# Kernel tuning notes

Hardware: AMD Instinct MI355X
Metric: run time of the kernel (lower is better)

## Reference

```python
import jax, jax.numpy as jnp
import numpy as np

N, E, IN_FT, OUT_FT = 8192, 4096, 512, 512
DENSITY = 0.02


def setup_inputs() -> dict:
    key = jax.random.key(0)
    k1, k2, k3, k4 = jax.random.split(key, 4)
    x = jax.random.normal(k1, (N, IN_FT), dtype=jnp.float32)
    hypergraph = (jax.random.uniform(k2, (N, E)) < DENSITY).astype(jnp.float32)
    # kaiming_uniform on [in, out]: fan_in = in_ft (torch fan of a Linear-style 2D param is dim 1 size? torch computes fan_in = size(1) for 2D -> out_ft here)
    bound_w = float(np.sqrt(6.0 / OUT_FT))  # kaiming_uniform a=sqrt(5)? default a=0 -> gain sqrt(2); bound = gain*sqrt(3/fan_in)
    bound_w = float(np.sqrt(2.0) * np.sqrt(3.0 / OUT_FT))
    weight = jax.random.uniform(k3, (IN_FT, OUT_FT), minval=-bound_w, maxval=bound_w, dtype=jnp.float32)
    bound_v = float(np.sqrt(2.0) * np.sqrt(3.0 / 1.0))
    V = jax.random.uniform(k4, (IN_FT, 1), minval=-bound_v, maxval=bound_v, dtype=jnp.float32)
    bias = jnp.zeros((OUT_FT,), dtype=jnp.float32)
    return {"x": x, "hypergraph": hypergraph, "weight": weight, "V": V, "bias": bias}


def reference(x, hypergraph, weight, V, bias):
    # edge embeddings: H^T @ x  -> [E, in_ft]
    edge_emb = hypergraph.T @ x
    hw = jax.nn.sigmoid(edge_emb @ V)          # [E, 1] learned hyperedge weights
    w = hw[:, 0]                                # [E]
    deg_v = (hypergraph @ hw)[:, 0]             # [N]  (sum over last dim of H @ hw)
    deg_e = jnp.sum(hypergraph, axis=0)         # [E]
    # adj = diag(deg_v) @ H @ diag(w) @ diag(deg_e) @ H^T @ diag(deg_v)
    # fused as broadcasted row/col scalings around two GEMMs (same math, no NxN)
    out = x @ weight                            # [N, out_ft]
    t = hypergraph.T @ (deg_v[:, None] * out)   # [E, out_ft]
    t = (w * deg_e)[:, None] * t                # diagonal edge scalings
    out = deg_v[:, None] * (hypergraph @ t)     # [N, out_ft]
    out = out + bias
    return (out, w)
```

## Files before the change

kernel.cpp:

```cpp
#include <hip/hip_runtime.h>


#define N_NODES 8192
#define N_EDGES 4096
#define FT 512

typedef short bf16x8 __attribute__((ext_vector_type(8)));
typedef float f32x4 __attribute__((ext_vector_type(4)));
typedef unsigned short u16;
typedef unsigned int u32;

__device__ __forceinline__ u16 f2b(float f) {
    union { float f; u32 u; } v; v.f = f;
    u32 r = v.u + 0x7FFFu + ((v.u >> 16) & 1u);
    return (u16)(r >> 16);
}
__device__ __forceinline__ float b2f(u16 h) {
    union { u32 u; float f; } v; v.u = ((u32)h) << 16; return v.f;
}


__global__ __launch_bounds__(256) void zero_kernel(float* p, int n) {
    int i = blockIdx.x * 256 + threadIdx.x;
    if (i < n) p[i] = 0.f;
}

__global__ __launch_bounds__(256) void xv_xb_kernel(const float* __restrict__ x,
                                                    const float* __restrict__ V,
                                                    float* __restrict__ xv,
                                                    u16* __restrict__ xb) {
    int row = blockIdx.x * 4 + (threadIdx.x >> 6);
    int lane = threadIdx.x & 63;
    const float* xr = x + (size_t)row * FT + lane * 8;
    const float* vr = V + lane * 8;
    float4 a0 = *(const float4*)xr, a1 = *(const float4*)(xr + 4);
    float4 b0 = *(const float4*)vr, b1 = *(const float4*)(vr + 4);
    float acc = a0.x * b0.x + a0.y * b0.y + a0.z * b0.z + a0.w * b0.w +
                a1.x * b1.x + a1.y * b1.y + a1.z * b1.z + a1.w * b1.w;
    u16 tmp[8] = {f2b(a0.x), f2b(a0.y), f2b(a0.z), f2b(a0.w),
                  f2b(a1.x), f2b(a1.y), f2b(a1.z), f2b(a1.w)};
    *(uint4*)(xb + (size_t)row * FT + lane * 8) = *(uint4*)tmp;
#pragma unroll
    for (int off = 32; off; off >>= 1) acc += __shfl_down(acc, off);
    if (lane == 0) xv[row] = acc;
}

__global__ __launch_bounds__(256) void prep_h4_kernel(const float* __restrict__ H,
                                                      const float* __restrict__ xv,
                                                      u16* __restrict__ Hbf,
                                                      u16* __restrict__ HTbf,
                                                      float* __restrict__ zsum,
                                                      float* __restrict__ desum) {
    __shared__ u32 Wt[64][33];
    __shared__ float xvs[64];
    const int t = threadIdx.x;
    const int e0 = blockIdx.x * 64, n0 = blockIdx.y * 64;
    if (t < 64) xvs[t] = xv[n0 + t];
    const int n_ld = t >> 2, seg = t & 3;
    u32 o[8];
    {
        const float* src = H + (size_t)(n0 + n_ld) * N_EDGES + e0 + seg * 16;
#pragma unroll
        for (int j = 0; j < 4; j++) {
            float4 h = *(const float4*)(src + j * 4);
            o[2 * j]     = (h.x != 0.f ? 0x3F80u : 0u) | (h.y != 0.f ? 0x3F800000u : 0u);
            o[2 * j + 1] = (h.z != 0.f ? 0x3F80u : 0u) | (h.w != 0.f ? 0x3F800000u : 0u);
        }
#pragma unroll
        for (int j = 0; j < 8; j++) Wt[n_ld][seg * 8 + j] = o[j];
    }
    __syncthreads();
    {
        u16* hdst = Hbf + (size_t)(n0 + n_ld) * N_EDGES + e0 + seg * 16;
        *(uint4*)hdst       = *(uint4*)&o[0];
        *(uint4*)(hdst + 8) = *(uint4*)&o[4];
    }
    {
        int e = t >> 2, g = t & 3;
        int ew = e >> 1;
        u32 sel = (e & 1) ? 0x07060302u : 0x05040100u;
        u32 oo[8];
        float z = 0.f, d = 0.f;
#pragma unroll
        for (int j = 0; j < 8; j++) {
            int np = g * 8 + j;
            oo[j] = __builtin_amdgcn_perm(Wt[2 * np + 1][ew], Wt[2 * np][ew], sel);
            z += (oo[j] & 0xFFFFu) ? xvs[2 * np] : 0.f;
            d += (oo[j] & 0xFFFFu) ? 1.f : 0.f;
            z += (oo[j] >> 16) ? xvs[2 * np + 1] : 0.f;
            d += (oo[j] >> 16) ? 1.f : 0.f;
        }
        u32* drow = (u32*)(HTbf + (size_t)(e0 + e) * N_NODES + n0);
        *(uint4*)(drow + g * 8)     = *(uint4*)&oo[0];
        *(uint4*)(drow + g * 8 + 4) = *(uint4*)&oo[4];
        z += __shfl_down(z, 2); z += __shfl_down(z, 1);
        d += __shfl_down(d, 2); d += __shfl_down(d, 1);
        if (g == 0) {
            atomicAdd(zsum + e0 + e, z);
            atomicAdd(desum + e0 + e, d);
        }
    }
}

__global__ __launch_bounds__(256) void sigmoid_kernel(const float* __restrict__ zsum,
                                                      const float* __restrict__ desum,
                                                      float* __restrict__ w_out,
                                                      float* __restrict__ wde) {
    int e = blockIdx.x * 256 + threadIdx.x;
    float z = zsum[e];
    float wv = 1.f / (1.f + expf(-z));
    w_out[e] = wv;
    wde[e] = wv * desum[e];
}

__global__ __launch_bounds__(256) void degv_kernel(const u16* __restrict__ Hbf,
                                                   const float* __restrict__ w,
                                                   float* __restrict__ degv) {
    int row = blockIdx.x * 4 + (threadIdx.x >> 6);
    int lane = threadIdx.x & 63;
    const uint4* hr = (const uint4*)(Hbf + (size_t)row * N_EDGES);
    float acc = 0.f;
#pragma unroll
    for (int i = 0; i < 8; i++) {
        int idx = i * 64 + lane;
        uint4 h = hr[idx];
        const float* w8 = w + idx * 8;
        float4 wa = *(const float4*)w8, wb = *(const float4*)(w8 + 4);
        acc += (h.x & 0xFFFFu) ? wa.x : 0.f;  acc += (h.x >> 16) ? wa.y : 0.f;
        acc += (h.y & 0xFFFFu) ? wa.z : 0.f;  acc += (h.y >> 16) ? wa.w : 0.f;
        acc += (h.z & 0xFFFFu) ? wb.x : 0.f;  acc += (h.z >> 16) ? wb.y : 0.f;
        acc += (h.w & 0xFFFFu) ? wb.z : 0.f;  acc += (h.w >> 16) ? wb.w : 0.f;
    }
#pragma unroll
    for (int off = 32; off; off >>= 1) acc += __shfl_down(acc, off);
    if (lane == 0) degv[row] = acc;
}

__global__ void wt_kernel(const float* __restrict__ src, u16* __restrict__ dst) {
    __shared__ float tile[32][33];
    int tx = threadIdx.x, ty = threadIdx.y;
    int c = blockIdx.x * 32 + tx;
    int r0 = blockIdx.y * 32;
#pragma unroll
    for (int i = 0; i < 4; i++)
        tile[ty + i * 8][tx] = src[(size_t)(r0 + ty + i * 8) * FT + c];
    __syncthreads();
#pragma unroll
    for (int i = 0; i < 4; i++)
        dst[(size_t)(blockIdx.x * 32 + ty + i * 8) * FT + r0 + tx] = f2b(tile[tx][ty + i * 8]);
}

__global__ void t2t_kernel(const u16* __restrict__ P, const float* __restrict__ wde,
                           u16* __restrict__ t2T) {
    __shared__ float tile[32][33];
    int tx = threadIdx.x, ty = threadIdx.y;
    int f0 = blockIdx.x * 32, e0 = blockIdx.y * 32;
#pragma unroll
    for (int i = 0; i < 4; i++) {
        int e = e0 + ty + i * 8;
        size_t idx = (size_t)e * 512 + f0 + tx;
        float s = 0.f;
#pragma unroll
        for (int sl = 0; sl < 8; sl++)
            s += b2f(P[idx + (size_t)sl * N_EDGES * 512]);
        tile[ty + i * 8][tx] = wde[e] * s;
    }
    __syncthreads();
#pragma unroll
    for (int i = 0; i < 4; i++)
        t2T[(size_t)(f0 + ty + i * 8) * N_EDGES + e0 + tx] = f2b(tile[tx][ty + i * 8]);
}

__global__ __launch_bounds__(256) void final_kernel(const u16* __restrict__ P,
                                                    const float* __restrict__ degv,
                                                    const float* __restrict__ bias,
                                                    float* __restrict__ out) {
    int i8 = blockIdx.x * 256 + threadIdx.x;
    int base = i8 * 8;
    int n = base >> 9, f = base & 511;
    float s[8] = {0.f, 0.f, 0.f, 0.f, 0.f, 0.f, 0.f, 0.f};
#pragma unroll
    for (int sl = 0; sl < 4; sl++) {
        uint4 v = *(const uint4*)(P + (size_t)sl * N_NODES * 512 + base);
        u32 ws[4] = {v.x, v.y, v.z, v.w};
#pragma unroll
        for (int j = 0; j < 4; j++) {
            s[2 * j]     += b2f((u16)(ws[j] & 0xFFFFu));
            s[2 * j + 1] += b2f((u16)(ws[j] >> 16));
        }
    }
    float dv = degv[n];
    float4 o0, o1;
    o0.x = dv * s[0] + bias[f + 0]; o0.y = dv * s[1] + bias[f + 1];
    o0.z = dv * s[2] + bias[f + 2]; o0.w = dv * s[3] + bias[f + 3];
    o1.x = dv * s[4] + bias[f + 4]; o1.y = dv * s[5] + bias[f + 5];
    o1.z = dv * s[6] + bias[f + 6]; o1.w = dv * s[7] + bias[f + 7];
    *(float4*)(out + base) = o0;
    *(float4*)(out + base + 4) = o1;
}


#define TBK 64

template <int MT, int NT, int EPI>
__global__ __launch_bounds__(256, 4)
void gemm9(const u16* __restrict__ Ap, const u16* __restrict__ Bp,
           void* __restrict__ Cp, const float* __restrict__ degv,
           int KC, int lda, int ldb, int ldc, size_t Ssz) {
    __shared__ __align__(16) u16 Alds[MT * 32 * TBK];
    __shared__ __align__(16) u16 Blds[NT * 32 * TBK];
    const int t = threadIdx.x;
    const int m0 = blockIdx.x * (MT * 32), n0 = blockIdx.y * (NT * 32);
    const int kbase = blockIdx.z * KC;
    const int wave = t >> 6, lane = t & 63, quad = lane >> 4, lo = lane & 15;
    const int wm = (wave >> 1) * (MT * 16), wn = (wave & 1) * (NT * 16);

    f32x4 acc[MT][NT];
#pragma unroll
    for (int a = 0; a < MT; a++)
#pragma unroll
        for (int b = 0; b < NT; b++) acc[a][b] = (f32x4){0.f, 0.f, 0.f, 0.f};

    for (int kk = 0; kk < KC; kk += TBK) {
        const int k0 = kbase + kk;
        __syncthreads();
#pragma unroll
        for (int i = 0; i < MT; i++) {
            int c = t + i * 256;
            int r = c >> 3;
            int j = ((c & 7) - r) & 7;
            const u16* g = Ap + (size_t)(m0 + r) * lda + k0 + j * 8;
            __builtin_amdgcn_global_load_lds((const u32*)g, (u32*)(Alds + c * 8), 16, 0, 0);
        }
#pragma unroll
        for (int i = 0; i < NT; i++) {
            int c = t + i * 256;
            int r = c >> 3;
            int j = ((c & 7) - r) & 7;
            const u16* g = Bp + (size_t)(n0 + r) * ldb + k0 + j * 8;
            __builtin_amdgcn_global_load_lds((const u32*)g, (u32*)(Blds + c * 8), 16, 0, 0);
        }
        __syncthreads();

#pragma unroll
        for (int s2 = 0; s2 < 2; s2++) {
            bf16x8 af[MT], bfr[NT];
#pragma unroll
            for (int mt = 0; mt < MT; mt++) {
                int m = wm + mt * 16 + lo;
                int s = (s2 * 4 + quad + m) & 7;
                af[mt] = *(const bf16x8*)&Alds[m * TBK + s * 8];
            }
#pragma unroll
            for (int nt = 0; nt < NT; nt++) {
                int n = wn + nt * 16 + lo;
                int s = (s2 * 4 + quad + n) & 7;
                bfr[nt] = *(const bf16x8*)&Blds[n * TBK + s * 8];
            }
#pragma unroll
            for (int mt = 0; mt < MT; mt++)
#pragma unroll
                for (int nt = 0; nt < NT; nt++)
                    acc[mt][nt] = __builtin_amdgcn_mfma_f32_16x16x32_bf16(af[mt], bfr[nt], acc[mt][nt], 0, 0, 0);
        }
    }

    if (EPI == 0) {
        u16* C = (u16*)Cp + (size_t)blockIdx.z * Ssz;
#pragma unroll
        for (int mt = 0; mt < MT; mt++) {
            int rb = m0 + wm + mt * 16 + quad * 4;
#pragma unroll
            for (int i = 0; i < 4; i++)
#pragma unroll
                for (int nt = 0; nt < NT; nt++)
                    C[(size_t)(rb + i) * ldc + n0 + wn + nt * 16 + lo] = f2b(acc[mt][nt][i]);
        }
    } else {
        u16* C = (u16*)Cp;
        float dv[NT];
#pragma unroll
        for (int nt = 0; nt < NT; nt++) dv[nt] = degv[n0 + wn + nt * 16 + lo];
#pragma unroll
        for (int mt = 0; mt < MT; mt++) {
            int rb = m0 + wm + mt * 16 + quad * 4;
#pragma unroll
            for (int i = 0; i < 4; i++)
#pragma unroll
                for (int nt = 0; nt < NT; nt++)
                    C[(size_t)(rb + i) * ldc + n0 + wn + nt * 16 + lo] =
                        f2b(acc[mt][nt][i] * dv[nt]);
        }
    }
}


extern "C" void kernel_launch(void* const* d_in, const int* in_sizes, int n_in,
                              void* d_out, int out_size, void* d_ws, size_t ws_size,
                              hipStream_t stream) {
    const float* x    = (const float*)d_in[0];
    const float* H    = (const float*)d_in[1];
    const float* W    = (const float*)d_in[2];
    const float* V    = (const float*)d_in[3];
    const float* bias = (const float*)d_in[4];
    float* out  = (float*)d_out;
    float* wout = out + (size_t)N_NODES * FT;
    (void)in_sizes; (void)n_in; (void)out_size; (void)ws_size;

    char* wsb = (char*)d_ws;
    float* wsf   = (float*)d_ws;
    float* xv    = wsf;
    float* zsum  = wsf + 8192;
    float* desum = wsf + 12288;
    float* degv  = wsf + 16384;
    float* wde   = wsf + 24576;
    u16*   Hbf   = (u16*)(wsb + 114688);
    u16*   HTbf  = (u16*)(wsb + 67223552);
    u16*   WT    = (u16*)(wsb + 134332416);
    u16*   doutT = (u16*)(wsb + 134856704);
    u16*   t2T   = (u16*)(wsb + 143245312);
    u16*   xb    = (u16*)(wsb + 147439616);
    u16*   P     = (u16*)(wsb + 155828224);

    zero_kernel<<<32, 256, 0, stream>>>(zsum, 8192);
    xv_xb_kernel<<<N_NODES / 4, 256, 0, stream>>>(x, V, xv, xb);
    prep_h4_kernel<<<dim3(N_EDGES / 64, N_NODES / 64), 256, 0, stream>>>(
        H, xv, Hbf, HTbf, zsum, desum);
    sigmoid_kernel<<<N_EDGES / 256, 256, 0, stream>>>(zsum, desum, wout, wde);
    degv_kernel<<<N_NODES / 4, 256, 0, stream>>>(Hbf, wout, degv);
    wt_kernel<<<dim3(16, 16), dim3(32, 8), 0, stream>>>(W, WT);

    gemm9<2, 4, 1><<<dim3(FT / 64, N_NODES / 128, 1), 256, 0, stream>>>(
        WT, xb, doutT, degv, FT, FT, FT, N_NODES, 0);

    gemm9<4, 4, 0><<<dim3(N_EDGES / 128, FT / 128, 8), 256, 0, stream>>>(
        HTbf, doutT, P, nullptr, N_NODES / 8, N_NODES, N_NODES, 512, (size_t)N_EDGES * 512);

    t2t_kernel<<<dim3(FT / 32, N_EDGES / 32), dim3(32, 8), 0, stream>>>(P, wde, t2T);

    gemm9<4, 4, 0><<<dim3(N_NODES / 128, FT / 128, 4), 256, 0, stream>>>(
        Hbf, t2T, P, nullptr, N_EDGES / 4, N_EDGES, N_EDGES, 512, (size_t)N_NODES * 512);

    final_kernel<<<(N_NODES * FT / 8) / 256, 256, 0, stream>>>(P, degv, bias, out);
}
```

Before: 354.3 us.

## Fuse small prep kernels and drop split-K in final GEMM with fused epilogue

Folds the zeroing into xv_xb_kernel and merges the sigmoid and weight-transpose kernels into one launch, cutting three launches. The last GEMM no longer splits K four ways into bf16 partials followed by a reduction kernel. It now runs the full K=4096 per block with a smaller 64-row tile and writes fp32 output directly with degree scaling and bias in the epilogue. This removes the partial-sum round trip through memory and one launch, but leaves fewer blocks (512) each doing a longer K loop.

```diff
diff --git a/kernel.cpp b/kernel.cpp
--- a/kernel.cpp
+++ b/kernel.cpp
@@ -20,15 +20,12 @@
 }
 
 
-__global__ __launch_bounds__(256) void zero_kernel(float* p, int n) {
-    int i = blockIdx.x * 256 + threadIdx.x;
-    if (i < n) p[i] = 0.f;
-}
-
 __global__ __launch_bounds__(256) void xv_xb_kernel(const float* __restrict__ x,
                                                     const float* __restrict__ V,
                                                     float* __restrict__ xv,
-                                                    u16* __restrict__ xb) {
+                                                    u16* __restrict__ xb,
+                                                    float* __restrict__ zd) {
+    if (blockIdx.x < 32) zd[blockIdx.x * 256 + threadIdx.x] = 0.f;
     int row = blockIdx.x * 4 + (threadIdx.x >> 6);
     int lane = threadIdx.x & 63;
     const float* xr = x + (size_t)row * FT + lane * 8;
@@ -102,15 +99,34 @@
     }
 }
 
-__global__ __launch_bounds__(256) void sigmoid_kernel(const float* __restrict__ zsum,
-                                                      const float* __restrict__ desum,
-                                                      float* __restrict__ w_out,
-                                                      float* __restrict__ wde) {
-    int e = blockIdx.x * 256 + threadIdx.x;
-    float z = zsum[e];
-    float wv = 1.f / (1.f + expf(-z));
-    w_out[e] = wv;
-    wde[e] = wv * desum[e];
+__global__ __launch_bounds__(256) void sigwt_kernel(const float* __restrict__ zsum,
+                                                    const float* __restrict__ desum,
+                                                    float* __restrict__ w_out,
+                                                    float* __restrict__ wde,
+                                                    const float* __restrict__ W,
+                                                    u16* __restrict__ WT) {
+    __shared__ float tile[32][33];
+    int bx = blockIdx.x;
+    if (bx < 16) {
+        int e = bx * 256 + threadIdx.x;
+        float z = zsum[e];
+        float wv = 1.f / (1.f + expf(-z));
+        w_out[e] = wv;
+        wde[e] = wv * desum[e];
+    } else {
+        int b = bx - 16;
+        int bxx = b & 15, byy = b >> 4;
+        int tx = threadIdx.x & 31, ty = threadIdx.x >> 5;
+        int c = bxx * 32 + tx;
+        int r0 = byy * 32;
+#pragma unroll
+        for (int i = 0; i < 4; i++)
+            tile[ty + i * 8][tx] = W[(size_t)(r0 + ty + i * 8) * FT + c];
+        __syncthreads();
+#pragma unroll
+        for (int i = 0; i < 4; i++)
+            WT[(size_t)(bxx * 32 + ty + i * 8) * FT + r0 + tx] = f2b(tile[tx][ty + i * 8]);
+    }
 }
 
 __global__ __launch_bounds__(256) void degv_kernel(const u16* __restrict__ Hbf,
@@ -136,20 +152,6 @@
     if (lane == 0) degv[row] = acc;
 }
 
-__global__ void wt_kernel(const float* __restrict__ src, u16* __restrict__ dst) {
-    __shared__ float tile[32][33];
-    int tx = threadIdx.x, ty = threadIdx.y;
-    int c = blockIdx.x * 32 + tx;
-    int r0 = blockIdx.y * 32;
-#pragma unroll
-    for (int i = 0; i < 4; i++)
-        tile[ty + i * 8][tx] = src[(size_t)(r0 + ty + i * 8) * FT + c];
-    __syncthreads();
-#pragma unroll
-    for (int i = 0; i < 4; i++)
-        dst[(size_t)(blockIdx.x * 32 + ty + i * 8) * FT + r0 + tx] = f2b(tile[tx][ty + i * 8]);
-}
-
 __global__ void t2t_kernel(const u16* __restrict__ P, const float* __restrict__ wde,
                            u16* __restrict__ t2T) {
     __shared__ float tile[32][33];
@@ -171,34 +173,6 @@
         t2T[(size_t)(f0 + ty + i * 8) * N_EDGES + e0 + tx] = f2b(tile[tx][ty + i * 8]);
 }
 
-__global__ __launch_bounds__(256) void final_kernel(const u16* __restrict__ P,
-                                                    const float* __restrict__ degv,
-                                                    const float* __restrict__ bias,
-                                                    float* __restrict__ out) {
-    int i8 = blockIdx.x * 256 + threadIdx.x;
-    int base = i8 * 8;
-    int n = base >> 9, f = base & 511;
-    float s[8] = {0.f, 0.f, 0.f, 0.f, 0.f, 0.f, 0.f, 0.f};
-#pragma unroll
-    for (int sl = 0; sl < 4; sl++) {
-        uint4 v = *(const uint4*)(P + (size_t)sl * N_NODES * 512 + base);
-        u32 ws[4] = {v.x, v.y, v.z, v.w};
-#pragma unroll
-        for (int j = 0; j < 4; j++) {
-            s[2 * j]     += b2f((u16)(ws[j] & 0xFFFFu));
-            s[2 * j + 1] += b2f((u16)(ws[j] >> 16));
-        }
-    }
-    float dv = degv[n];
-    float4 o0, o1;
-    o0.x = dv * s[0] + bias[f + 0]; o0.y = dv * s[1] + bias[f + 1];
-    o0.z = dv * s[2] + bias[f + 2]; o0.w = dv * s[3] + bias[f + 3];
-    o1.x = dv * s[4] + bias[f + 4]; o1.y = dv * s[5] + bias[f + 5];
-    o1.z = dv * s[6] + bias[f + 6]; o1.w = dv * s[7] + bias[f + 7];
-    *(float4*)(out + base) = o0;
-    *(float4*)(out + base + 4) = o1;
-}
-
 
 #define TBK 64
 
@@ -206,6 +180,7 @@
 __global__ __launch_bounds__(256, 4)
 void gemm9(const u16* __restrict__ Ap, const u16* __restrict__ Bp,
            void* __restrict__ Cp, const float* __restrict__ degv,
+           const float* __restrict__ bias,
            int KC, int lda, int ldb, int ldc, size_t Ssz) {
     __shared__ __align__(16) u16 Alds[MT * 32 * TBK];
     __shared__ __align__(16) u16 Blds[NT * 32 * TBK];
@@ -276,7 +251,7 @@
                 for (int nt = 0; nt < NT; nt++)
                     C[(size_t)(rb + i) * ldc + n0 + wn + nt * 16 + lo] = f2b(acc[mt][nt][i]);
         }
-    } else {
+    } else if (EPI == 1) {
         u16* C = (u16*)Cp;
         float dv[NT];
 #pragma unroll
@@ -290,6 +265,23 @@
                 for (int nt = 0; nt < NT; nt++)
                     C[(size_t)(rb + i) * ldc + n0 + wn + nt * 16 + lo] =
                         f2b(acc[mt][nt][i] * dv[nt]);
+        }
+    } else {
+        float* C = (float*)Cp;
+        float bs[NT];
+#pragma unroll
+        for (int nt = 0; nt < NT; nt++) bs[nt] = bias[n0 + wn + nt * 16 + lo];
+#pragma unroll
+        for (int mt = 0; mt < MT; mt++) {
+            int rb = m0 + wm + mt * 16 + quad * 4;
+#pragma unroll
+            for (int i = 0; i < 4; i++) {
+                float dvv = degv[rb + i];
+#pragma unroll
+                for (int nt = 0; nt < NT; nt++)
+                    C[(size_t)(rb + i) * ldc + n0 + wn + nt * 16 + lo] =
+                        acc[mt][nt][i] * dvv + bs[nt];
+            }
         }
     }
 }
@@ -322,24 +314,21 @@
     u16*   xb    = (u16*)(wsb + 147439616);
     u16*   P     = (u16*)(wsb + 155828224);
 
-    zero_kernel<<<32, 256, 0, stream>>>(zsum, 8192);
-    xv_xb_kernel<<<N_NODES / 4, 256, 0, stream>>>(x, V, xv, xb);
+    xv_xb_kernel<<<N_NODES / 4, 256, 0, stream>>>(x, V, xv, xb, zsum);
     prep_h4_kernel<<<dim3(N_EDGES / 64, N_NODES / 64), 256, 0, stream>>>(
         H, xv, Hbf, HTbf, zsum, desum);
-    sigmoid_kernel<<<N_EDGES / 256, 256, 0, stream>>>(zsum, desum, wout, wde);
+    sigwt_kernel<<<16 + 256, 256, 0, stream>>>(zsum, desum, wout, wde, W, WT);
     degv_kernel<<<N_NODES / 4, 256, 0, stream>>>(Hbf, wout, degv);
-    wt_kernel<<<dim3(16, 16), dim3(32, 8), 0, stream>>>(W, WT);
 
     gemm9<2, 4, 1><<<dim3(FT / 64, N_NODES / 128, 1), 256, 0, stream>>>(
-        WT, xb, doutT, degv, FT, FT, FT, N_NODES, 0);
+        WT, xb, doutT, degv, nullptr, FT, FT, FT, N_NODES, 0);
 
     gemm9<4, 4, 0><<<dim3(N_EDGES / 128, FT / 128, 8), 256, 0, stream>>>(
-        HTbf, doutT, P, nullptr, N_NODES / 8, N_NODES, N_NODES, 512, (size_t)N_EDGES * 512);
+        HTbf, doutT, P, nullptr, nullptr, N_NODES / 8, N_NODES, N_NODES, 512,
+        (size_t)N_EDGES * 512);
 
     t2t_kernel<<<dim3(FT / 32, N_EDGES / 32), dim3(32, 8), 0, stream>>>(P, wde, t2T);
 
-    gemm9<4, 4, 0><<<dim3(N_NODES / 128, FT / 128, 4), 256, 0, stream>>>(
-        Hbf, t2T, P, nullptr, N_EDGES / 4, N_EDGES, N_EDGES, 512, (size_t)N_NODES * 512);
-
-    final_kernel<<<(N_NODES * FT / 8) / 256, 256, 0, stream>>>(P, degv, bias, out);
-}
+    gemm9<2, 4, 2><<<dim3(N_NODES / 64, FT / 128, 1), 256, 0, stream>>>(
+        Hbf, t2T, out, degv, bias, N_EDGES, N_EDGES, N_EDGES, FT, 0);
+}
```

Measured after the change: 367.5 us. +3.7%, slower.

## Merge small launches and enlarge prep tile to 128x128

Applied to the files above, without the earlier changes.

Folds the zsum/desum zeroing into the xv/xb kernel and merges the sigmoid and weight-transpose kernels into one launch, cutting the kernel count by two. The H conversion/transpose kernel now processes 128x128 tiles with 64 elements per thread instead of 64x64, which halves the number of atomics and blocks and lengthens each thread's contiguous writes. The trade-off is more registers and LDS per block (about 33KB), which may lower occupancy in what is a bandwidth-bound pass over the 128MB H matrix.

```diff
diff --git a/kernel.cpp b/kernel.cpp
--- a/kernel.cpp
+++ b/kernel.cpp
@@ -20,15 +20,12 @@
 }
 
 
-__global__ __launch_bounds__(256) void zero_kernel(float* p, int n) {
-    int i = blockIdx.x * 256 + threadIdx.x;
-    if (i < n) p[i] = 0.f;
-}
-
 __global__ __launch_bounds__(256) void xv_xb_kernel(const float* __restrict__ x,
                                                     const float* __restrict__ V,
                                                     float* __restrict__ xv,
-                                                    u16* __restrict__ xb) {
+                                                    u16* __restrict__ xb,
+                                                    float* __restrict__ zd) {
+    if (blockIdx.x < 32) zd[blockIdx.x * 256 + threadIdx.x] = 0.f;
     int row = blockIdx.x * 4 + (threadIdx.x >> 6);
     int lane = threadIdx.x & 63;
     const float* xr = x + (size_t)row * FT + lane * 8;
@@ -45,56 +42,58 @@
     if (lane == 0) xv[row] = acc;
 }
 
-__global__ __launch_bounds__(256) void prep_h4_kernel(const float* __restrict__ H,
+__global__ __launch_bounds__(256) void prep_h5_kernel(const float* __restrict__ H,
                                                       const float* __restrict__ xv,
                                                       u16* __restrict__ Hbf,
                                                       u16* __restrict__ HTbf,
                                                       float* __restrict__ zsum,
                                                       float* __restrict__ desum) {
-    __shared__ u32 Wt[64][33];
-    __shared__ float xvs[64];
+    __shared__ u32 Wt[128][65];
+    __shared__ float xvs[128];
     const int t = threadIdx.x;
-    const int e0 = blockIdx.x * 64, n0 = blockIdx.y * 64;
-    if (t < 64) xvs[t] = xv[n0 + t];
-    const int n_ld = t >> 2, seg = t & 3;
-    u32 o[8];
+    const int e0 = blockIdx.x * 128, n0 = blockIdx.y * 128;
+    if (t < 128) xvs[t] = xv[n0 + t];
+    const int r = t >> 1, h = t & 1;
+    u32 o[32];
     {
-        const float* src = H + (size_t)(n0 + n_ld) * N_EDGES + e0 + seg * 16;
-#pragma unroll
-        for (int j = 0; j < 4; j++) {
-            float4 h = *(const float4*)(src + j * 4);
-            o[2 * j]     = (h.x != 0.f ? 0x3F80u : 0u) | (h.y != 0.f ? 0x3F800000u : 0u);
-            o[2 * j + 1] = (h.z != 0.f ? 0x3F80u : 0u) | (h.w != 0.f ? 0x3F800000u : 0u);
-        }
-#pragma unroll
-        for (int j = 0; j < 8; j++) Wt[n_ld][seg * 8 + j] = o[j];
+        const float* src = H + (size_t)(n0 + r) * N_EDGES + e0 + h * 64;
+#pragma unroll
+        for (int j = 0; j < 16; j++) {
+            float4 v = *(const float4*)(src + j * 4);
+            o[2 * j]     = (v.x != 0.f ? 0x3F80u : 0u) | (v.y != 0.f ? 0x3F800000u : 0u);
+            o[2 * j + 1] = (v.z != 0.f ? 0x3F80u : 0u) | (v.w != 0.f ? 0x3F800000u : 0u);
+        }
+#pragma unroll
+        for (int k = 0; k < 32; k++) Wt[r][h * 32 + k] = o[k];
     }
     __syncthreads();
     {
-        u16* hdst = Hbf + (size_t)(n0 + n_ld) * N_EDGES + e0 + seg * 16;
-        *(uint4*)hdst       = *(uint4*)&o[0];
-        *(uint4*)(hdst + 8) = *(uint4*)&o[4];
+        u16* hdst = Hbf + (size_t)(n0 + r) * N_EDGES + e0 + h * 64;
+#pragma unroll
+        for (int k = 0; k < 8; k++)
+            *(uint4*)(hdst + k * 8) = *(uint4*)&o[k * 4];
     }
     {
-        int e = t >> 2, g = t & 3;
-        int ew = e >> 1;
-        u32 sel = (e & 1) ? 0x07060302u : 0x05040100u;
-        u32 oo[8];
+        const int e = t >> 1, g = t & 1;
+        const int ew = e >> 1;
+        const u32 sel = (e & 1) ? 0x07060302u : 0x05040100u;
+        u32 oo[32];
         float z = 0.f, d = 0.f;
 #pragma unroll
-        for (int j = 0; j < 8; j++) {
-            int np = g * 8 + j;
+        for (int j = 0; j < 32; j++) {
+            int np = g * 32 + j;
             oo[j] = __builtin_amdgcn_perm(Wt[2 * np + 1][ew], Wt[2 * np][ew], sel);
             z += (oo[j] & 0xFFFFu) ? xvs[2 * np] : 0.f;
             d += (oo[j] & 0xFFFFu) ? 1.f : 0.f;
             z += (oo[j] >> 16) ? xvs[2 * np + 1] : 0.f;
             d += (oo[j] >> 16) ? 1.f : 0.f;
         }
-        u32* drow = (u32*)(HTbf + (size_t)(e0 + e) * N_NODES + n0);
-        *(uint4*)(drow + g * 8)     = *(uint4*)&oo[0];
-        *(uint4*)(drow + g * 8 + 4) = *(uint4*)&oo[4];
-        z += __shfl_down(z, 2); z += __shfl_down(z, 1);
-        d += __shfl_down(d, 2); d += __shfl_down(d, 1);
+        u16* drow = HTbf + (size_t)(e0 + e) * N_NODES + n0 + g * 64;
+#pragma unroll
+        for (int k = 0; k < 8; k++)
+            *(uint4*)(drow + k * 8) = *(uint4*)&oo[k * 4];
+        z += __shfl_down(z, 1);
+        d += __shfl_down(d, 1);
         if (g == 0) {
             atomicAdd(zsum + e0 + e, z);
             atomicAdd(desum + e0 + e, d);
@@ -102,15 +101,34 @@
     }
 }
 
-__global__ __launch_bounds__(256) void sigmoid_kernel(const float* __restrict__ zsum,
-                                                      const float* __restrict__ desum,
-                                                      float* __restrict__ w_out,
-                                                      float* __restrict__ wde) {
-    int e = blockIdx.x * 256 + threadIdx.x;
-    float z = zsum[e];
-    float wv = 1.f / (1.f + expf(-z));
-    w_out[e] = wv;
-    wde[e] = wv * desum[e];
+__global__ __launch_bounds__(256) void sigwt_kernel(const float* __restrict__ zsum,
+                                                    const float* __restrict__ desum,
+                                                    float* __restrict__ w_out,
+                                                    float* __restrict__ wde,
+                                                    const float* __restrict__ W,
+                                                    u16* __restrict__ WT) {
+    __shared__ float tile[32][33];
+    int bx = blockIdx.x;
+    if (bx < 16) {
+        int e = bx * 256 + threadIdx.x;
+        float z = zsum[e];
+        float wv = 1.f / (1.f + expf(-z));
+        w_out[e] = wv;
+        wde[e] = wv * desum[e];
+    } else {
+        int b = bx - 16;
+        int bxx = b & 15, byy = b >> 4;
+        int tx = threadIdx.x & 31, ty = threadIdx.x >> 5;
+        int c = bxx * 32 + tx;
+        int r0 = byy * 32;
+#pragma unroll
+        for (int i = 0; i < 4; i++)
+            tile[ty + i * 8][tx] = W[(size_t)(r0 + ty + i * 8) * FT + c];
+        __syncthreads();
+#pragma unroll
+        for (int i = 0; i < 4; i++)
+            WT[(size_t)(bxx * 32 + ty + i * 8) * FT + r0 + tx] = f2b(tile[tx][ty + i * 8]);
+    }
 }
 
 __global__ __launch_bounds__(256) void degv_kernel(const u16* __restrict__ Hbf,
@@ -134,20 +152,6 @@
 #pragma unroll
     for (int off = 32; off; off >>= 1) acc += __shfl_down(acc, off);
     if (lane == 0) degv[row] = acc;
-}
-
-__global__ void wt_kernel(const float* __restrict__ src, u16* __restrict__ dst) {
-    __shared__ float tile[32][33];
-    int tx = threadIdx.x, ty = threadIdx.y;
-    int c = blockIdx.x * 32 + tx;
-    int r0 = blockIdx.y * 32;
-#pragma unroll
-    for (int i = 0; i < 4; i++)
-        tile[ty + i * 8][tx] = src[(size_t)(r0 + ty + i * 8) * FT + c];
-    __syncthreads();
-#pragma unroll
-    for (int i = 0; i < 4; i++)
-        dst[(size_t)(blockIdx.x * 32 + ty + i * 8) * FT + r0 + tx] = f2b(tile[tx][ty + i * 8]);
 }
 
 __global__ void t2t_kernel(const u16* __restrict__ P, const float* __restrict__ wde,
@@ -322,13 +326,11 @@
     u16*   xb    = (u16*)(wsb + 147439616);
     u16*   P     = (u16*)(wsb + 155828224);
 
-    zero_kernel<<<32, 256, 0, stream>>>(zsum, 8192);
-    xv_xb_kernel<<<N_NODES / 4, 256, 0, stream>>>(x, V, xv, xb);
-    prep_h4_kernel<<<dim3(N_EDGES / 64, N_NODES / 64), 256, 0, stream>>>(
+    xv_xb_kernel<<<N_NODES / 4, 256, 0, stream>>>(x, V, xv, xb, zsum);
+    prep_h5_kernel<<<dim3(N_EDGES / 128, N_NODES / 128), 256, 0, stream>>>(
         H, xv, Hbf, HTbf, zsum, desum);
-    sigmoid_kernel<<<N_EDGES / 256, 256, 0, stream>>>(zsum, desum, wout, wde);
+    sigwt_kernel<<<16 + 256, 256, 0, stream>>>(zsum, desum, wout, wde, W, WT);
     degv_kernel<<<N_NODES / 4, 256, 0, stream>>>(Hbf, wout, degv);
-    wt_kernel<<<dim3(16, 16), dim3(32, 8), 0, stream>>>(W, WT);
 
     gemm9<2, 4, 1><<<dim3(FT / 64, N_NODES / 128, 1), 256, 0, stream>>>(
         WT, xb, doutT, degv, FT, FT, FT, N_NODES, 0);
```

Measured after the change: 360.6 us. About the same (+1.8%).

## Pad leading dimensions of bf16 operand matrices and merge small prep kernels

Applied to the files above, without the earlier changes.

Adds padded row strides (+32 elements) for Hbf, HTbf, doutT and t2T and passes them to the GEMMs. The padding is meant to avoid channel or bank conflicts caused by power-of-two strides. It also folds the zeroing into xv_xb_kernel and merges the sigmoid and weight-transpose kernels into one launch to cut launch overhead. The cost is a slightly larger workspace and new offsets that must stay consistent.

```diff
diff --git a/kernel.cpp b/kernel.cpp
--- a/kernel.cpp
+++ b/kernel.cpp
@@ -4,6 +4,10 @@
 #define N_NODES 8192
 #define N_EDGES 4096
 #define FT 512
+#define LDH  4128
+#define LDHT 8224
+#define LDD  8224
+#define LDT  4128
 
 typedef short bf16x8 __attribute__((ext_vector_type(8)));
 typedef float f32x4 __attribute__((ext_vector_type(4)));
@@ -20,15 +24,12 @@
 }
 
 
-__global__ __launch_bounds__(256) void zero_kernel(float* p, int n) {
-    int i = blockIdx.x * 256 + threadIdx.x;
-    if (i < n) p[i] = 0.f;
-}
-
 __global__ __launch_bounds__(256) void xv_xb_kernel(const float* __restrict__ x,
                                                     const float* __restrict__ V,
                                                     float* __restrict__ xv,
-                                                    u16* __restrict__ xb) {
+                                                    u16* __restrict__ xb,
+                                                    float* __restrict__ zd) {
+    if (blockIdx.x < 32) zd[blockIdx.x * 256 + threadIdx.x] = 0.f;
     int row = blockIdx.x * 4 + (threadIdx.x >> 6);
     int lane = threadIdx.x & 63;
     const float* xr = x + (size_t)row * FT + lane * 8;
@@ -71,7 +72,7 @@
     }
     __syncthreads();
     {
-        u16* hdst = Hbf + (size_t)(n0 + n_ld) * N_EDGES + e0 + seg * 16;
+        u16* hdst = Hbf + (size_t)(n0 + n_ld) * LDH + e0 + seg * 16;
         *(uint4*)hdst       = *(uint4*)&o[0];
         *(uint4*)(hdst + 8) = *(uint4*)&o[4];
     }
@@ -90,7 +91,7 @@
             z += (oo[j] >> 16) ? xvs[2 * np + 1] : 0.f;
             d += (oo[j] >> 16) ? 1.f : 0.f;
         }
-        u32* drow = (u32*)(HTbf + (size_t)(e0 + e) * N_NODES + n0);
+        u32* drow = (u32*)(HTbf + (size_t)(e0 + e) * LDHT + n0);
         *(uint4*)(drow + g * 8)     = *(uint4*)&oo[0];
         *(uint4*)(drow + g * 8 + 4) = *(uint4*)&oo[4];
         z += __shfl_down(z, 2); z += __shfl_down(z, 1);
@@ -102,15 +103,34 @@
     }
 }
 
-__global__ __launch_bounds__(256) void sigmoid_kernel(const float* __restrict__ zsum,
-                                                      const float* __restrict__ desum,
-                                                      float* __restrict__ w_out,
-                                                      float* __restrict__ wde) {
-    int e = blockIdx.x * 256 + threadIdx.x;
-    float z = zsum[e];
-    float wv = 1.f / (1.f + expf(-z));
-    w_out[e] = wv;
-    wde[e] = wv * desum[e];
+__global__ __launch_bounds__(256) void sigwt_kernel(const float* __restrict__ zsum,
+                                                    const float* __restrict__ desum,
+                                                    float* __restrict__ w_out,
+                                                    float* __restrict__ wde,
+                                                    const float* __restrict__ W,
+                                                    u16* __restrict__ WT) {
+    __shared__ float tile[32][33];
+    int bx = blockIdx.x;
+    if (bx < 16) {
+        int e = bx * 256 + threadIdx.x;
+        float z = zsum[e];
+        float wv = 1.f / (1.f + expf(-z));
+        w_out[e] = wv;
+        wde[e] = wv * desum[e];
+    } else {
+        int b = bx - 16;
+        int bxx = b & 15, byy = b >> 4;
+        int tx = threadIdx.x & 31, ty = threadIdx.x >> 5;
+        int c = bxx * 32 + tx;
+        int r0 = byy * 32;
+#pragma unroll
+        for (int i = 0; i < 4; i++)
+            tile[ty + i * 8][tx] = W[(size_t)(r0 + ty + i * 8) * FT + c];
+        __syncthreads();
+#pragma unroll
+        for (int i = 0; i < 4; i++)
+            WT[(size_t)(bxx * 32 + ty + i * 8) * FT + r0 + tx] = f2b(tile[tx][ty + i * 8]);
+    }
 }
 
 __global__ __launch_bounds__(256) void degv_kernel(const u16* __restrict__ Hbf,
@@ -118,7 +138,7 @@
                                                    float* __restrict__ degv) {
     int row = blockIdx.x * 4 + (threadIdx.x >> 6);
     int lane = threadIdx.x & 63;
-    const uint4* hr = (const uint4*)(Hbf + (size_t)row * N_EDGES);
+    const uint4* hr = (const uint4*)(Hbf + (size_t)row * LDH);
     float acc = 0.f;
 #pragma unroll
     for (int i = 0; i < 8; i++) {
@@ -136,20 +156,6 @@
     if (lane == 0) degv[row] = acc;
 }
 
-__global__ void wt_kernel(const float* __restrict__ src, u16* __restrict__ dst) {
-    __shared__ float tile[32][33];
-    int tx = threadIdx.x, ty = threadIdx.y;
-    int c = blockIdx.x * 32 + tx;
-    int r0 = blockIdx.y * 32;
-#pragma unroll
-    for (int i = 0; i < 4; i++)
-        tile[ty + i * 8][tx] = src[(size_t)(r0 + ty + i * 8) * FT + c];
-    __syncthreads();
-#pragma unroll
-    for (int i = 0; i < 4; i++)
-        dst[(size_t)(blockIdx.x * 32 + ty + i * 8) * FT + r0 + tx] = f2b(tile[tx][ty + i * 8]);
-}
-
 __global__ void t2t_kernel(const u16* __restrict__ P, const float* __restrict__ wde,
                            u16* __restrict__ t2T) {
     __shared__ float tile[32][33];
@@ -168,7 +174,7 @@
     __syncthreads();
 #pragma unroll
     for (int i = 0; i < 4; i++)
-        t2T[(size_t)(f0 + ty + i * 8) * N_EDGES + e0 + tx] = f2b(tile[tx][ty + i * 8]);
+        t2T[(size_t)(f0 + ty + i * 8) * LDT + e0 + tx] = f2b(tile[tx][ty + i * 8]);
 }
 
 __global__ __launch_bounds__(256) void final_kernel(const u16* __restrict__ P,
@@ -315,31 +321,29 @@
     float* degv  = wsf + 16384;
     float* wde   = wsf + 24576;
     u16*   Hbf   = (u16*)(wsb + 114688);
-    u16*   HTbf  = (u16*)(wsb + 67223552);
-    u16*   WT    = (u16*)(wsb + 134332416);
-    u16*   doutT = (u16*)(wsb + 134856704);
-    u16*   t2T   = (u16*)(wsb + 143245312);
-    u16*   xb    = (u16*)(wsb + 147439616);
-    u16*   P     = (u16*)(wsb + 155828224);
-
-    zero_kernel<<<32, 256, 0, stream>>>(zsum, 8192);
-    xv_xb_kernel<<<N_NODES / 4, 256, 0, stream>>>(x, V, xv, xb);
+    u16*   HTbf  = (u16*)(wsb + 67747840);
+    u16*   WT    = (u16*)(wsb + 135118848);
+    u16*   doutT = (u16*)(wsb + 135643136);
+    u16*   t2T   = (u16*)(wsb + 144064512);
+    u16*   xb    = (u16*)(wsb + 148291584);
+    u16*   P     = (u16*)(wsb + 156680192);
+
+    xv_xb_kernel<<<N_NODES / 4, 256, 0, stream>>>(x, V, xv, xb, zsum);
     prep_h4_kernel<<<dim3(N_EDGES / 64, N_NODES / 64), 256, 0, stream>>>(
         H, xv, Hbf, HTbf, zsum, desum);
-    sigmoid_kernel<<<N_EDGES / 256, 256, 0, stream>>>(zsum, desum, wout, wde);
+    sigwt_kernel<<<16 + 256, 256, 0, stream>>>(zsum, desum, wout, wde, W, WT);
     degv_kernel<<<N_NODES / 4, 256, 0, stream>>>(Hbf, wout, degv);
-    wt_kernel<<<dim3(16, 16), dim3(32, 8), 0, stream>>>(W, WT);
 
     gemm9<2, 4, 1><<<dim3(FT / 64, N_NODES / 128, 1), 256, 0, stream>>>(
-        WT, xb, doutT, degv, FT, FT, FT, N_NODES, 0);
+        WT, xb, doutT, degv, FT, FT, FT, LDD, 0);
 
     gemm9<4, 4, 0><<<dim3(N_EDGES / 128, FT / 128, 8), 256, 0, stream>>>(
-        HTbf, doutT, P, nullptr, N_NODES / 8, N_NODES, N_NODES, 512, (size_t)N_EDGES * 512);
+        HTbf, doutT, P, nullptr, N_NODES / 8, LDHT, LDD, 512, (size_t)N_EDGES * 512);
 
     t2t_kernel<<<dim3(FT / 32, N_EDGES / 32), dim3(32, 8), 0, stream>>>(P, wde, t2T);
 
     gemm9<4, 4, 0><<<dim3(N_NODES / 128, FT / 128, 4), 256, 0, stream>>>(
-        Hbf, t2T, P, nullptr, N_EDGES / 4, N_EDGES, N_EDGES, 512, (size_t)N_NODES * 512);
+        Hbf, t2T, P, nullptr, N_EDGES / 4, LDH, LDT, 512, (size_t)N_NODES * 512);
 
     final_kernel<<<(N_NODES * FT / 8) / 256, 256, 0, stream>>>(P, degv, bias, out);
 }
```

Result: slower. 393.0 us (+10.9%).
